# Performance work log

Hardware: AMD Instinct MI355X
Metric: run time of the kernel (lower is better)

## Reference

```python
import jax, jax.numpy as jnp
import numpy as np

EPS = 1e-5

def layernorm(x, w, b):
    m = jnp.mean(x, axis=-1, keepdims=True)
    v = jnp.var(x, axis=-1, keepdims=True)
    return (x - m) * jax.lax.rsqrt(v + EPS) * w + b

def setup_inputs() -> dict:
    key = jax.random.key(0)
    ks = jax.random.split(key, 20)
    B, N, D, H, C = 4, 2048, 512, 8, 3
    HID = int(D * 4.0 * (2.0 / 3.0))  # SwiGLU hidden = 1365
    g = lambda k, shape, s: (jax.random.normal(k, shape, jnp.float32) * s)
    return {
        "x": g(ks[0], (B, N, D), 1.0),
        "coords": jax.random.uniform(ks[1], (B, N, C), jnp.float32),
        "ln1_w": jnp.ones((D,), jnp.float32),
        "ln1_b": jnp.zeros((D,), jnp.float32),
        "ln2_w": jnp.ones((D,), jnp.float32),
        "ln2_b": jnp.zeros((D,), jnp.float32),
        "Wqkv": g(ks[2], (D, 3 * D), D ** -0.5),
        "bqkv": jnp.zeros((3 * D,), jnp.float32),
        "Wo": g(ks[3], (D, D), D ** -0.5),
        "bo": jnp.zeros((D,), jnp.float32),
        "Wc": g(ks[4], (C, H), 0.1),
        "bc": jnp.zeros((H,), jnp.float32),
        "W1": g(ks[5], (D, HID), D ** -0.5),
        "b1": jnp.zeros((HID,), jnp.float32),
        "W2": g(ks[6], (D, HID), D ** -0.5),
        "b2": jnp.zeros((HID,), jnp.float32),
        "W3": g(ks[7], (HID, D), HID ** -0.5),
        "b3": jnp.zeros((D,), jnp.float32),
    }

def reference(x, coords, ln1_w, ln1_b, ln2_w, ln2_b, Wqkv, bqkv, Wo, bo,
              Wc, bc, W1, b1, W2, b2, W3, b3):
    B, N, D = x.shape
    H = bc.shape[0]
    dh = D // H
    # --- coord-aware patch attention (pre-norm) ---
    h = layernorm(x, ln1_w, ln1_b)
    qkv = h @ Wqkv + bqkv                                # [B,N,3D]
    q, k, v = jnp.split(qkv, 3, axis=-1)
    to_heads = lambda t: t.reshape(B, N, H, dh).transpose(0, 2, 1, 3)  # [B,H,N,dh]
    q, k, v = to_heads(q), to_heads(k), to_heads(v)
    scores = jnp.einsum("bhnd,bhmd->bhnm", q, k) / np.sqrt(dh)
    rel = coords[:, :, None, :] - coords[:, None, :, :]  # [B,N,N,C]
    bias = jnp.einsum("bnmc,ch->bhnm", rel, Wc) + bc[None, :, None, None]
    attn = jax.nn.softmax(scores + bias, axis=-1)
    o = jnp.einsum("bhnm,bhmd->bhnd", attn, v)
    o = o.transpose(0, 2, 1, 3).reshape(B, N, D)
    x = x + (o @ Wo + bo)                                # residual 1
    # --- SwiGLU FFN (pre-norm) ---
    h2 = layernorm(x, ln2_w, ln2_b)
    ff = jax.nn.silu(h2 @ W1 + b1) * (h2 @ W2 + b2)
    x = x + (ff @ W3 + b3)                               # residual 2
    return x
```

## Files before the change

kernel.cpp:

```cpp
#include <hip/hip_runtime.h>
#include <hip/hip_bf16.h>
#include <math.h>

#define B_   4
#define N_   2048
#define D_   512
#define H_   8
#define DH_  64
#define C_   3
#define HID_ 1365
#define HIDP 1408
#define ROWS_ (B_*N_)
#define TD_  (3*D_)

typedef __attribute__((ext_vector_type(8))) short short8;
typedef __attribute__((ext_vector_type(4))) float floatx4;
typedef __attribute__((ext_vector_type(2))) unsigned uint2v;

#define MFMA16(a,b,c) __builtin_amdgcn_mfma_f32_16x16x32_bf16(a,b,c,0,0,0)

typedef __attribute__((address_space(3))) unsigned lds_u32;
typedef __attribute__((address_space(1))) unsigned glb_u32;

__device__ __forceinline__ short sh(float v){
  union { __hip_bfloat16 b; short s; } u;
  u.b = __float2bfloat16(v);
  return u.s;
}

__device__ __forceinline__ unsigned pk2(float a, float b){
  union { short s[2]; unsigned u; } z;
  z.s[0] = sh(a); z.s[1] = sh(b);
  return z.u;
}

__device__ __forceinline__ int swz(int col, int row){
  return (col & ~63) | (col & 7) | ((((col >> 3) & 7) ^ (row & 7)) << 3);
}

template<int ROWS, int PITCH, int WAVES = 4>
__device__ __forceinline__ void stageG(short* __restrict__ lds,
    const short* __restrict__ g, int ldg, int t){
  const int LPR = PITCH/8;
  const int RPI = 64/LPR;
  const int PW  = (ROWS/RPI)/WAVES;
  int lane = t & 63, w = t >> 6;
  #pragma unroll
  for (int i = 0; i < PW; ++i){
    int r0  = (w*PW + i)*RPI;
    int row = r0 + lane/LPR;
    const short* ga = g + (size_t)row*ldg + (lane % LPR)*8;
    short* la = lds + r0*PITCH;
    __builtin_amdgcn_global_load_lds((const glb_u32*)ga, (lds_u32*)la, 16, 0, 0);
  }
}

__device__ __forceinline__ short8 fragS(const short* __restrict__ lds, int pitch,
    int mbase, int lane, int kk){
  int row  = mbase + (lane & 15);
  int seg  = (kk >> 3) + (lane >> 4);
  int phys = seg ^ (row & 7);
  return *(const short8*)(lds + row*pitch + phys*8);
}

__global__ __launch_bounds__(256) void convT_all(
    const float* __restrict__ Wqkv, const float* __restrict__ Wo,
    const float* __restrict__ W1, const float* __restrict__ W2,
    const float* __restrict__ W3,
    short* __restrict__ Wtqkv, short* __restrict__ Wto,
    short* __restrict__ Wt1, short* __restrict__ Wt2, short* __restrict__ Wt3,
    const float* __restrict__ coords, const float* __restrict__ Wc,
    float* __restrict__ tv,
    const float* __restrict__ x, const float* __restrict__ ln1_w,
    const float* __restrict__ ln1_b, short* __restrict__ h){
  int id = blockIdx.x;
  int t = threadIdx.x;
  if (id >= 3392){
    int row = id - 3392;
    size_t base = (size_t)row * D_;
    float2 u = *(const float2*)&x[base + 2*t];
    float s  = u.x + u.y;
    float s2 = u.x*u.x + u.y*u.y;
    #pragma unroll
    for (int off = 32; off >= 1; off >>= 1){
      s  += __shfl_xor(s,  off, 64);
      s2 += __shfl_xor(s2, off, 64);
    }
    __shared__ float red[8];
    int lane = t & 63, wv = t >> 6;
    if (lane == 0){ red[wv] = s; red[4+wv] = s2; }
    __syncthreads();
    float sum  = red[0]+red[1]+red[2]+red[3];
    float sum2 = red[4]+red[5]+red[6]+red[7];
    float mean = sum * (1.0f/D_);
    float var  = sum2 * (1.0f/D_) - mean*mean;
    float inv  = rsqrtf(fmaxf(var, 0.f) + 1e-5f);
    float2 wv2 = *(const float2*)&ln1_w[2*t];
    float2 bv2 = *(const float2*)&ln1_b[2*t];
    *(unsigned*)(h + base + swz(2*t, row)) =
        pk2((u.x-mean)*inv*wv2.x + bv2.x, (u.y-mean)*inv*wv2.y + bv2.y);
    return;
  }
  if (id >= 3136){
    int idx = (id - 3136)*256 + t;
    int n = idx & (N_-1);
    int hh = (idx >> 11) & (H_-1);
    int b = idx >> 14;
    float s = 0.f;
    #pragma unroll
    for (int cc = 0; cc < C_; ++cc)
      s += coords[((size_t)(b*N_+n))*C_ + cc] * Wc[cc*H_ + hh];
    tv[idx] = s * 1.44269504f;
    return;
  }
  __shared__ float tile[32][33];
  const float* in; short* out; int K, NN, Kp, nx;
  if (id < 768)      { in=Wqkv; out=Wtqkv; K=512;  NN=1536; Kp=512;  nx=48; }
  else if (id < 1024){ in=Wo;   out=Wto;   K=512;  NN=512;  Kp=512;  nx=16; id-=768; }
  else if (id < 1728){ in=W1;   out=Wt1;   K=512;  NN=HID_; Kp=512;  nx=44; id-=1024; }
  else if (id < 2432){ in=W2;   out=Wt2;   K=512;  NN=HID_; Kp=512;  nx=44; id-=1728; }
  else               { in=W3;   out=Wt3;   K=HID_; NN=512;  Kp=HIDP; nx=16; id-=2432; }
  int nt0 = (id % nx)*32, kt0 = (id / nx)*32;
  int r = t >> 5, cc = t & 31;
  #pragma unroll
  for (int i=0;i<4;++i){
    int k = kt0 + i*8 + r, n = nt0 + cc;
    tile[i*8+r][cc] = (k<K && n<NN) ? in[(size_t)k*NN + n] : 0.f;
  }
  __syncthreads();
  #pragma unroll
  for (int i=0;i<4;++i){
    int n = nt0 + i*8 + r, k = kt0 + cc;
    out[(size_t)n*Kp + swz(k, n)] = sh(tile[cc][i*8+r]);
  }
}

__global__ __launch_bounds__(256) void ln_kernel(const float* __restrict__ x,
        const float* __restrict__ w, const float* __restrict__ b,
        short* __restrict__ out){
  int row = blockIdx.x;
  size_t base = (size_t)row * D_;
  int t = threadIdx.x;
  float2 u = *(const float2*)&x[base + 2*t];
  float s  = u.x + u.y;
  float s2 = u.x*u.x + u.y*u.y;
  #pragma unroll
  for (int off = 32; off >= 1; off >>= 1){
    s  += __shfl_xor(s,  off, 64);
    s2 += __shfl_xor(s2, off, 64);
  }
  __shared__ float red[8];
  int lane = t & 63, wv = t >> 6;
  if (lane == 0){ red[wv] = s; red[4+wv] = s2; }
  __syncthreads();
  float sum  = red[0]+red[1]+red[2]+red[3];
  float sum2 = red[4]+red[5]+red[6]+red[7];
  float mean = sum * (1.0f/D_);
  float var  = sum2 * (1.0f/D_) - mean*mean;
  float inv  = rsqrtf(fmaxf(var, 0.f) + 1e-5f);
  float2 wv2 = *(const float2*)&w[2*t];
  float2 bv2 = *(const float2*)&b[2*t];
  *(unsigned*)(out + base + swz(2*t, row)) =
      pk2((u.x-mean)*inv*wv2.x + bv2.x, (u.y-mean)*inv*wv2.y + bv2.y);
}

__global__ __launch_bounds__(256) void qkv_gemm(
    const short* __restrict__ A, const short* __restrict__ Bt,
    const float* __restrict__ bias,
    short* __restrict__ qb, short* __restrict__ kb, short* __restrict__ vbt){
  __shared__ short As[2][128*64];
  __shared__ short Bs[2][128*64];
  int t = threadIdx.x;
  int lane = t & 63, w = t >> 6;
  int wr = (w >> 1) * 64, wc = (w & 1) * 64;
  int col0 = blockIdx.x * 128, row0 = blockIdx.y * 128;
  bool vblk = (blockIdx.x >= 8);
  floatx4 acc[4][4];
  #pragma unroll
  for (int mt=0;mt<4;++mt)
    #pragma unroll
    for (int nt=0;nt<4;++nt) acc[mt][nt] = (floatx4){0.f,0.f,0.f,0.f};
  stageG<128,64>(As[0], A  + (size_t)row0*D_, D_, t);
  stageG<128,64>(Bs[0], Bt + (size_t)col0*D_, D_, t);
  for (int ti = 0; ti < 8; ++ti){
    int cur = ti & 1;
    __syncthreads();
    if (ti + 1 < 8){
      stageG<128,64>(As[cur^1], A  + (size_t)row0*D_ + (ti+1)*64, D_, t);
      stageG<128,64>(Bs[cur^1], Bt + (size_t)col0*D_ + (ti+1)*64, D_, t);
    }
    #pragma unroll
    for (int kk = 0; kk < 64; kk += 32){
      short8 af[4], bf[4];
      #pragma unroll
      for (int mt=0;mt<4;++mt) af[mt] = fragS(As[cur], 64, wr+mt*16, lane, kk);
      #pragma unroll
      for (int nt=0;nt<4;++nt) bf[nt] = fragS(Bs[cur], 64, wc+nt*16, lane, kk);
      if (vblk){
        #pragma unroll
        for (int mt=0;mt<4;++mt)
          #pragma unroll
          for (int nt=0;nt<4;++nt)
            acc[mt][nt] = MFMA16(af[mt], bf[nt], acc[mt][nt]);
      } else {
        #pragma unroll
        for (int mt=0;mt<4;++mt)
          #pragma unroll
          for (int nt=0;nt<4;++nt)
            acc[mt][nt] = MFMA16(bf[nt], af[mt], acc[mt][nt]);
      }
    }
  }
  int quad = lane >> 4, c = lane & 15;
  if (vblk){
    #pragma unroll
    for (int mt=0;mt<4;++mt){
      int rb0 = row0 + wr + mt*16 + quad*4;
      int bidx = rb0 >> 11, n0 = rb0 & (N_-1);
      #pragma unroll
      for (int nt=0;nt<4;++nt){
        int col = col0 + wc + nt*16 + c;
        int d = col & (D_-1), hh = d >> 6, hd = d & 63;
        float bc = bias[col];
        uint2v pv;
        pv.x = pk2(acc[mt][nt][0]+bc, acc[mt][nt][1]+bc);
        pv.y = pk2(acc[mt][nt][2]+bc, acc[mt][nt][3]+bc);
        *(uint2v*)(vbt + (((size_t)(bidx*H_ + hh))*DH_ + hd)*N_ + swz(n0, hd)) = pv;
      }
    }
  } else {
    #pragma unroll
    for (int mt=0;mt<4;++mt){
      int row = row0 + wr + mt*16 + c;
      int bidx = row >> 11, n = row & (N_-1);
      #pragma unroll
      for (int nt=0;nt<4;++nt){
        int d0 = col0 + wc + nt*16 + quad*4;
        floatx4 b4 = *(const floatx4*)&bias[d0];
        int which = d0 >> 9, dd = d0 & (D_-1), hh = dd >> 6, hd0 = dd & 63;
        short* dst = which ? kb : qb;
        uint2v pv;
        pv.x = pk2(acc[mt][nt][0]+b4[0], acc[mt][nt][1]+b4[1]);
        pv.y = pk2(acc[mt][nt][2]+b4[2], acc[mt][nt][3]+b4[3]);
        *(uint2v*)(dst + (((size_t)(bidx*H_ + hh))*N_ + n)*DH_ + swz(hd0, n)) = pv;
      }
    }
  }
}

__global__ __launch_bounds__(256) void gemm64(
    const short* __restrict__ A, int lda,
    const short* __restrict__ Bt, int Ktot,
    const float* __restrict__ bias,
    const float* __restrict__ resid, float* __restrict__ outF){
  __shared__ short As[2][128*64];
  __shared__ short Bs[2][64*64];
  int t = threadIdx.x, lane = t & 63, w = t >> 6;
  int wr = w * 32;
  int col0 = blockIdx.x * 64, row0 = blockIdx.y * 128;
  floatx4 acc[2][4];
  #pragma unroll
  for (int mt=0;mt<2;++mt)
    #pragma unroll
    for (int nt=0;nt<4;++nt) acc[mt][nt] = (floatx4){0.f,0.f,0.f,0.f};
  stageG<128,64>(As[0], A  + (size_t)row0*lda, lda, t);
  stageG<64,64> (Bs[0], Bt + (size_t)col0*Ktot, Ktot, t);
  const int NT = Ktot >> 6;
  for (int ti = 0; ti < NT; ++ti){
    int cur = ti & 1;
    __syncthreads();
    if (ti + 1 < NT){
      stageG<128,64>(As[cur^1], A  + (size_t)row0*lda + (ti+1)*64, lda, t);
      stageG<64,64> (Bs[cur^1], Bt + (size_t)col0*Ktot + (ti+1)*64, Ktot, t);
    }
    #pragma unroll
    for (int kk = 0; kk < 64; kk += 32){
      short8 af[2], bf[4];
      #pragma unroll
      for (int mt=0;mt<2;++mt) af[mt] = fragS(As[cur], 64, wr+mt*16, lane, kk);
      #pragma unroll
      for (int nt=0;nt<4;++nt) bf[nt] = fragS(Bs[cur], 64, nt*16, lane, kk);
      #pragma unroll
      for (int mt=0;mt<2;++mt)
        #pragma unroll
        for (int nt=0;nt<4;++nt)
          acc[mt][nt] = MFMA16(bf[nt], af[mt], acc[mt][nt]);
    }
  }
  int quad = lane >> 4, c = lane & 15;
  #pragma unroll
  for (int mt=0;mt<2;++mt){
    int row = row0 + wr + mt*16 + c;
    #pragma unroll
    for (int nt=0;nt<4;++nt){
      int c0 = col0 + nt*16 + quad*4;
      size_t idx = (size_t)row*D_ + c0;
      float4 rv = *(const float4*)&resid[idx];
      floatx4 b4 = *(const floatx4*)&bias[c0];
      float4 ov;
      ov.x = acc[mt][nt][0] + b4[0] + rv.x;
      ov.y = acc[mt][nt][1] + b4[1] + rv.y;
      ov.z = acc[mt][nt][2] + b4[2] + rv.z;
      ov.w = acc[mt][nt][3] + b4[3] + rv.w;
      *(float4*)&outF[idx] = ov;
    }
  }
}

__global__ __launch_bounds__(256) void gate_gemm(
    const short* __restrict__ A,
    const short* __restrict__ Bt1, const short* __restrict__ Bt2,
    const float* __restrict__ b1, const float* __restrict__ b2,
    short* __restrict__ ff){
  __shared__ short As[128*64];
  __shared__ short B1s[64*64];
  __shared__ short B2s[64*64];
  int t = threadIdx.x, lane = t & 63, w = t >> 6;
  int wr = (w >> 1) * 64, wc = (w & 1) * 32;
  int col0 = blockIdx.x * 64, row0 = blockIdx.y * 128;
  floatx4 a1[4][2], a2[4][2];
  #pragma unroll
  for (int mt=0;mt<4;++mt)
    #pragma unroll
    for (int nt=0;nt<2;++nt){
      a1[mt][nt] = (floatx4){0.f,0.f,0.f,0.f};
      a2[mt][nt] = (floatx4){0.f,0.f,0.f,0.f};
    }
  for (int k0 = 0; k0 < D_; k0 += 64){
    __syncthreads();
    stageG<128,64>(As, A + (size_t)row0*D_ + k0, D_, t);
    stageG<64,64>(B1s, Bt1 + (size_t)col0*D_ + k0, D_, t);
    stageG<64,64>(B2s, Bt2 + (size_t)col0*D_ + k0, D_, t);
    __syncthreads();
    #pragma unroll
    for (int kk = 0; kk < 64; kk += 32){
      short8 af[4], f1[2], f2[2];
      #pragma unroll
      for (int mt=0;mt<4;++mt) af[mt] = fragS(As, 64, wr+mt*16, lane, kk);
      #pragma unroll
      for (int nt=0;nt<2;++nt){
        f1[nt] = fragS(B1s, 64, wc+nt*16, lane, kk);
        f2[nt] = fragS(B2s, 64, wc+nt*16, lane, kk);
      }
      #pragma unroll
      for (int mt=0;mt<4;++mt)
        #pragma unroll
        for (int nt=0;nt<2;++nt){
          a1[mt][nt] = MFMA16(f1[nt], af[mt], a1[mt][nt]);
          a2[mt][nt] = MFMA16(f2[nt], af[mt], a2[mt][nt]);
        }
    }
  }
  int quad = lane >> 4, c = lane & 15;
  #pragma unroll
  for (int mt=0;mt<4;++mt){
    int row = row0 + wr + mt*16 + c;
    size_t rbase = (size_t)row * HIDP;
    #pragma unroll
    for (int nt=0;nt<2;++nt){
      int c0 = col0 + wc + nt*16 + quad*4;
      float v[4];
      #pragma unroll
      for (int r=0;r<4;++r){
        int col = c0 + r;
        float g1 = a1[mt][nt][r] + (col < HID_ ? b1[col] : 0.f);
        float g2 = a2[mt][nt][r] + (col < HID_ ? b2[col] : 0.f);
        float sig = 1.f / (1.f + __expf(-g1));
        v[r] = g1*sig*g2;
      }
      uint2v pv;
      pv.x = pk2(v[0], v[1]);
      pv.y = pk2(v[2], v[3]);
      *(uint2v*)(ff + rbase + swz(c0, row)) = pv;
    }
  }
}

#define EXP2SC 0.18033688011112042f
__global__ __launch_bounds__(256) void attn_mfma(
    const short* __restrict__ qb, const short* __restrict__ kbuf,
    const short* __restrict__ vbt, const float* __restrict__ tv,
    short* __restrict__ o){
  __shared__ short Ks2[2][128*64];
  __shared__ short Vt2[2][64*128];
  __shared__ __align__(16) float tsAll[2048];
  int qt = blockIdx.x, h = blockIdx.y, b = blockIdx.z;
  int bh = b*H_ + h;
  int t = threadIdx.x, lane = t & 63, w = t >> 6;
  int quad = lane >> 4, c = lane & 15;
  const short* Kbase = kbuf + (size_t)bh*N_*DH_;
  const short* Vbase = vbt  + (size_t)bh*DH_*N_;

  #pragma unroll
  for (int i = 0; i < 2; ++i)
    *(floatx4*)&tsAll[t*8 + i*4] = *(const floatx4*)&tv[(size_t)bh*N_ + t*8 + i*4];
  stageG<128,64>(Ks2[1], qb + ((size_t)bh*N_ + qt*128)*DH_, DH_, t);
  stageG<128,64>(Ks2[0], Kbase, DH_, t);
  stageG<64,128>(Vt2[0], Vbase, N_, t);
  __syncthreads();
  short8 qf[2][2];
  #pragma unroll
  for (int mt=0;mt<2;++mt)
    #pragma unroll
    for (int kh=0;kh<2;++kh)
      qf[mt][kh] = fragS(Ks2[1], 64, w*32 + mt*16, lane, kh*32);
  floatx4 O[2][4];
  float l_i[2] = {0.f, 0.f};
  #pragma unroll
  for (int mt=0;mt<2;++mt)
    #pragma unroll
    for (int nt=0;nt<4;++nt) O[mt][nt] = (floatx4){0.f,0.f,0.f,0.f};
  __syncthreads();

  for (int kt = 0; kt < N_/128; ++kt){
    int cur = kt & 1;
    if (kt + 1 < N_/128){
      stageG<128,64>(Ks2[cur^1], Kbase + (size_t)(kt+1)*128*DH_, DH_, t);
      stageG<64,128>(Vt2[cur^1], Vbase + (kt+1)*128, N_, t);
    }
    const short* Kc  = Ks2[cur];
    const short* Vc  = Vt2[cur];
    const float* tsc = tsAll + kt*128;
    #pragma unroll
    for (int kb4 = 0; kb4 < 4; ++kb4){
      floatx4 St[2][2];
      #pragma unroll
      for (int i=0;i<2;++i){
        St[i][0] = (floatx4){0.f,0.f,0.f,0.f};
        St[i][1] = (floatx4){0.f,0.f,0.f,0.f};
      }
      #pragma unroll
      for (int kh=0;kh<2;++kh){
        short8 kf0 = fragS(Kc, 64, kb4*32,      lane, kh*32);
        short8 kf1 = fragS(Kc, 64, kb4*32 + 16, lane, kh*32);
        #pragma unroll
        for (int mt=0;mt<2;++mt){
          St[0][mt] = MFMA16(kf0, qf[mt][kh], St[0][mt]);
          St[1][mt] = MFMA16(kf1, qf[mt][kh], St[1][mt]);
        }
      }
      floatx4 t0 = *(const floatx4*)&tsc[kb4*32 + quad*4];
      floatx4 t1 = *(const floatx4*)&tsc[kb4*32 + 16 + quad*4];
      short8 pbf[2];
      #pragma unroll
      for (int mt=0;mt<2;++mt){
        float p0[4], p1[4];
        #pragma unroll
        for (int r=0;r<4;++r){
          p0[r] = __builtin_amdgcn_exp2f(fmaf(St[0][mt][r], EXP2SC, -t0[r]));
          p1[r] = __builtin_amdgcn_exp2f(fmaf(St[1][mt][r], EXP2SC, -t1[r]));
        }
        l_i[mt] += (p0[0]+p0[1]) + (p0[2]+p0[3]) + (p1[0]+p1[1]) + (p1[2]+p1[3]);
        unsigned X0 = pk2(p0[0], p0[1]), X1 = pk2(p0[2], p0[3]);
        unsigned Y0 = pk2(p1[0], p1[1]), Y1 = pk2(p1[2], p1[3]);
        auto u0 = __builtin_amdgcn_permlane32_swap(X0, Y0, false, false);
        auto v0 = __builtin_amdgcn_permlane16_swap(u0[0], u0[1], false, false);
        auto u1 = __builtin_amdgcn_permlane32_swap(X1, Y1, false, false);
        auto v1 = __builtin_amdgcn_permlane16_swap(u1[0], u1[1], false, false);
        union { short8 s; unsigned uu[4]; } pb;
        pb.uu[0] = v0[0]; pb.uu[1] = v1[0]; pb.uu[2] = v0[1]; pb.uu[3] = v1[1];
        pbf[mt] = pb.s;
      }
      #pragma unroll
      for (int nt=0;nt<4;++nt){
        short8 vf = fragS(Vc, 128, nt*16, lane, kb4*32);
        #pragma unroll
        for (int mt=0;mt<2;++mt)
          O[mt][nt] = MFMA16(vf, pbf[mt], O[mt][nt]);
      }
    }
    __syncthreads();
  }
  #pragma unroll
  for (int mt=0;mt<2;++mt){
    float l = l_i[mt];
    l += __shfl_xor(l, 16, 64);
    l += __shfl_xor(l, 32, 64);
    float invl = 1.f / l;
    int qrow = qt*128 + w*32 + mt*16 + c;
    size_t rb = ((size_t)b*N_ + qrow)*(size_t)D_;
    #pragma unroll
    for (int nt=0;nt<4;++nt){
      int d0 = h*DH_ + nt*16 + quad*4;
      uint2v pv;
      pv.x = pk2(O[mt][nt][0]*invl, O[mt][nt][1]*invl);
      pv.y = pk2(O[mt][nt][2]*invl, O[mt][nt][3]*invl);
      *(uint2v*)(o + rb + swz(d0, qrow)) = pv;
    }
  }
}

extern "C" void kernel_launch(void* const* d_in, const int* in_sizes, int n_in,
                              void* d_out, int out_size, void* d_ws, size_t ws_size,
                              hipStream_t stream){
  const float* x      = (const float*)d_in[0];
  const float* coords = (const float*)d_in[1];
  const float* ln1_w  = (const float*)d_in[2];
  const float* ln1_b  = (const float*)d_in[3];
  const float* ln2_w  = (const float*)d_in[4];
  const float* ln2_b  = (const float*)d_in[5];
  const float* Wqkv   = (const float*)d_in[6];
  const float* bqkv   = (const float*)d_in[7];
  const float* Wo     = (const float*)d_in[8];
  const float* bo     = (const float*)d_in[9];
  const float* Wc     = (const float*)d_in[10];
  const float* W1     = (const float*)d_in[12];
  const float* b1     = (const float*)d_in[13];
  const float* W2     = (const float*)d_in[14];
  const float* b2     = (const float*)d_in[15];
  const float* W3     = (const float*)d_in[16];
  const float* b3     = (const float*)d_in[17];

  char* ws = (char*)d_ws;
  short* Wtqkv = (short*)(ws);
  short* Wto   = (short*)(ws + 1572864);
  short* Wt1   = (short*)(ws + 2097152);
  short* Wt2   = (short*)(ws + 3538944);
  short* Wt3   = (short*)(ws + 4980736);
  float* tv    = (float*)(ws + 6422528);
  short* h     = (short*)(ws + 6684672);
  short* qb    = (short*)(ws + 15073280);
  short* kb    = (short*)(ws + 23461888);
  short* vbt   = (short*)(ws + 31850496);
  short* o     = h;
  short* h2    = h;
  short* ff    = qb;
  float* x1    = (float*)d_out;

  convT_all<<<dim3(11584), dim3(256), 0, stream>>>(Wqkv, Wo, W1, W2, W3,
      Wtqkv, Wto, Wt1, Wt2, Wt3, coords, Wc, tv, x, ln1_w, ln1_b, h);
  qkv_gemm<<<dim3(12,64), dim3(256), 0, stream>>>(h, Wtqkv, bqkv, qb, kb, vbt);
  attn_mfma<<<dim3(16,8,4), dim3(256), 0, stream>>>(qb, kb, vbt, tv, o);
  gemm64<<<dim3(8,64), dim3(256), 0, stream>>>(o, 512, Wto, 512, bo, x, x1);
  ln_kernel<<<dim3(ROWS_), dim3(256), 0, stream>>>(x1, ln2_w, ln2_b, h2);
  gate_gemm<<<dim3(22,64), dim3(256), 0, stream>>>(h2, Wt1, Wt2, b1, b2, ff);
  gemm64<<<dim3(8,64), dim3(256), 0, stream>>>(ff, HIDP, Wt3, HIDP, b3, x1, x1);
}
```

Baseline: 305.1 us.

## Remap workgroups for XCD-local L2 reuse and software-pipeline attention QK/PV

Flattens the launch grids of the QKV, output, gate and W3 GEMMs and of attention into 1D, then remaps block IDs so that consecutive tiles sharing rows or heads land on the same XCD. The intent is better L2 reuse across MI355X's per-XCD caches. The attention inner loop is also restructured to interleave the QK^T MFMAs of the next 32-key sub-block with the softmax/PV of the current one, so MFMA work overlaps exp and permute work. This raises live register pressure through two S accumulator sets.

After: 277.2 us. 1.1x faster.

```diff
diff --git a/kernel.cpp b/kernel.cpp
--- a/kernel.cpp
+++ b/kernel.cpp
@@ -36,6 +36,10 @@
 
 __device__ __forceinline__ int swz(int col, int row){
   return (col & ~63) | (col & 7) | ((((col >> 3) & 7) ^ (row & 7)) << 3);
+}
+
+__device__ __forceinline__ int xcdswz(int bid, int nwg){
+  return (bid & 7) * (nwg >> 3) + (bid >> 3);
 }
 
 template<int ROWS, int PITCH, int WAVES = 4>
@@ -173,8 +177,10 @@
   int t = threadIdx.x;
   int lane = t & 63, w = t >> 6;
   int wr = (w >> 1) * 64, wc = (w & 1) * 64;
-  int col0 = blockIdx.x * 128, row0 = blockIdx.y * 128;
-  bool vblk = (blockIdx.x >= 8);
+  int wg = xcdswz(blockIdx.x, 768);
+  int colblk = wg % 12, rowblk = wg / 12;
+  int col0 = colblk * 128, row0 = rowblk * 128;
+  bool vblk = (colblk >= 8);
   floatx4 acc[4][4];
   #pragma unroll
   for (int mt=0;mt<4;++mt)
@@ -257,7 +263,8 @@
   __shared__ short Bs[2][64*64];
   int t = threadIdx.x, lane = t & 63, w = t >> 6;
   int wr = w * 32;
-  int col0 = blockIdx.x * 64, row0 = blockIdx.y * 128;
+  int wg = xcdswz(blockIdx.x, 512);
+  int col0 = (wg & 7) * 64, row0 = (wg >> 3) * 128;
   floatx4 acc[2][4];
   #pragma unroll
   for (int mt=0;mt<2;++mt)
@@ -317,7 +324,8 @@
   __shared__ short B2s[64*64];
   int t = threadIdx.x, lane = t & 63, w = t >> 6;
   int wr = (w >> 1) * 64, wc = (w & 1) * 32;
-  int col0 = blockIdx.x * 64, row0 = blockIdx.y * 128;
+  int wg = xcdswz(blockIdx.x, 1408);
+  int col0 = (wg % 22) * 64, row0 = (wg / 22) * 128;
   floatx4 a1[4][2], a2[4][2];
   #pragma unroll
   for (int mt=0;mt<4;++mt)
@@ -377,6 +385,54 @@
 }
 
 #define EXP2SC 0.18033688011112042f
+
+#define ZERO_S(S) { \
+  S[0][0] = (floatx4){0.f,0.f,0.f,0.f}; S[0][1] = (floatx4){0.f,0.f,0.f,0.f}; \
+  S[1][0] = (floatx4){0.f,0.f,0.f,0.f}; S[1][1] = (floatx4){0.f,0.f,0.f,0.f}; }
+
+#define QKT(S, kb) { \
+  _Pragma("unroll") \
+  for (int kh=0;kh<2;++kh){ \
+    short8 kf0 = fragS(Kc, 64, (kb)*32,      lane, kh*32); \
+    short8 kf1 = fragS(Kc, 64, (kb)*32 + 16, lane, kh*32); \
+    _Pragma("unroll") \
+    for (int mt=0;mt<2;++mt){ \
+      S[0][mt] = MFMA16(kf0, qf[mt][kh], S[0][mt]); \
+      S[1][mt] = MFMA16(kf1, qf[mt][kh], S[1][mt]); \
+    } \
+  } }
+
+#define SOFTPV(S, kb) { \
+  floatx4 t0 = *(const floatx4*)&tsc[(kb)*32 + quad*4]; \
+  floatx4 t1 = *(const floatx4*)&tsc[(kb)*32 + 16 + quad*4]; \
+  short8 pbf[2]; \
+  _Pragma("unroll") \
+  for (int mt=0;mt<2;++mt){ \
+    float p0[4], p1[4]; \
+    _Pragma("unroll") \
+    for (int r=0;r<4;++r){ \
+      p0[r] = __builtin_amdgcn_exp2f(fmaf(S[0][mt][r], EXP2SC, -t0[r])); \
+      p1[r] = __builtin_amdgcn_exp2f(fmaf(S[1][mt][r], EXP2SC, -t1[r])); \
+    } \
+    l_i[mt] += (p0[0]+p0[1]) + (p0[2]+p0[3]) + (p1[0]+p1[1]) + (p1[2]+p1[3]); \
+    unsigned X0 = pk2(p0[0], p0[1]), X1 = pk2(p0[2], p0[3]); \
+    unsigned Y0 = pk2(p1[0], p1[1]), Y1 = pk2(p1[2], p1[3]); \
+    auto u0 = __builtin_amdgcn_permlane32_swap(X0, Y0, false, false); \
+    auto v0 = __builtin_amdgcn_permlane16_swap(u0[0], u0[1], false, false); \
+    auto u1 = __builtin_amdgcn_permlane32_swap(X1, Y1, false, false); \
+    auto v1 = __builtin_amdgcn_permlane16_swap(u1[0], u1[1], false, false); \
+    union { short8 s; unsigned uu[4]; } pb; \
+    pb.uu[0] = v0[0]; pb.uu[1] = v1[0]; pb.uu[2] = v0[1]; pb.uu[3] = v1[1]; \
+    pbf[mt] = pb.s; \
+  } \
+  _Pragma("unroll") \
+  for (int nt=0;nt<4;++nt){ \
+    short8 vf = fragS(Vc, 128, nt*16, lane, (kb)*32); \
+    _Pragma("unroll") \
+    for (int mt=0;mt<2;++mt) \
+      O[mt][nt] = MFMA16(vf, pbf[mt], O[mt][nt]); \
+  } }
+
 __global__ __launch_bounds__(256) void attn_mfma(
     const short* __restrict__ qb, const short* __restrict__ kbuf,
     const short* __restrict__ vbt, const float* __restrict__ tv,
@@ -384,8 +440,9 @@
   __shared__ short Ks2[2][128*64];
   __shared__ short Vt2[2][64*128];
   __shared__ __align__(16) float tsAll[2048];
-  int qt = blockIdx.x, h = blockIdx.y, b = blockIdx.z;
-  int bh = b*H_ + h;
+  int wg = xcdswz(blockIdx.x, 512);
+  int bh = wg >> 4, qt = wg & 15;
+  int b = bh >> 3, h = bh & 7;
   int t = threadIdx.x, lane = t & 63, w = t >> 6;
   int quad = lane >> 4, c = lane & 15;
   const short* Kbase = kbuf + (size_t)bh*N_*DH_;
@@ -421,54 +478,15 @@
     const short* Kc  = Ks2[cur];
     const short* Vc  = Vt2[cur];
     const float* tsc = tsAll + kt*128;
-    #pragma unroll
-    for (int kb4 = 0; kb4 < 4; ++kb4){
-      floatx4 St[2][2];
-      #pragma unroll
-      for (int i=0;i<2;++i){
-        St[i][0] = (floatx4){0.f,0.f,0.f,0.f};
-        St[i][1] = (floatx4){0.f,0.f,0.f,0.f};
-      }
-      #pragma unroll
-      for (int kh=0;kh<2;++kh){
-        short8 kf0 = fragS(Kc, 64, kb4*32,      lane, kh*32);
-        short8 kf1 = fragS(Kc, 64, kb4*32 + 16, lane, kh*32);
-        #pragma unroll
-        for (int mt=0;mt<2;++mt){
-          St[0][mt] = MFMA16(kf0, qf[mt][kh], St[0][mt]);
-          St[1][mt] = MFMA16(kf1, qf[mt][kh], St[1][mt]);
-        }
-      }
-      floatx4 t0 = *(const floatx4*)&tsc[kb4*32 + quad*4];
-      floatx4 t1 = *(const floatx4*)&tsc[kb4*32 + 16 + quad*4];
-      short8 pbf[2];
-      #pragma unroll
-      for (int mt=0;mt<2;++mt){
-        float p0[4], p1[4];
-        #pragma unroll
-        for (int r=0;r<4;++r){
-          p0[r] = __builtin_amdgcn_exp2f(fmaf(St[0][mt][r], EXP2SC, -t0[r]));
-          p1[r] = __builtin_amdgcn_exp2f(fmaf(St[1][mt][r], EXP2SC, -t1[r]));
-        }
-        l_i[mt] += (p0[0]+p0[1]) + (p0[2]+p0[3]) + (p1[0]+p1[1]) + (p1[2]+p1[3]);
-        unsigned X0 = pk2(p0[0], p0[1]), X1 = pk2(p0[2], p0[3]);
-        unsigned Y0 = pk2(p1[0], p1[1]), Y1 = pk2(p1[2], p1[3]);
-        auto u0 = __builtin_amdgcn_permlane32_swap(X0, Y0, false, false);
-        auto v0 = __builtin_amdgcn_permlane16_swap(u0[0], u0[1], false, false);
-        auto u1 = __builtin_amdgcn_permlane32_swap(X1, Y1, false, false);
-        auto v1 = __builtin_amdgcn_permlane16_swap(u1[0], u1[1], false, false);
-        union { short8 s; unsigned uu[4]; } pb;
-        pb.uu[0] = v0[0]; pb.uu[1] = v1[0]; pb.uu[2] = v0[1]; pb.uu[3] = v1[1];
-        pbf[mt] = pb.s;
-      }
-      #pragma unroll
-      for (int nt=0;nt<4;++nt){
-        short8 vf = fragS(Vc, 128, nt*16, lane, kb4*32);
-        #pragma unroll
-        for (int mt=0;mt<2;++mt)
-          O[mt][nt] = MFMA16(vf, pbf[mt], O[mt][nt]);
-      }
-    }
+    floatx4 Sa[2][2], Sb[2][2];
+    ZERO_S(Sa); QKT(Sa, 0);
+    ZERO_S(Sb); QKT(Sb, 1);
+    SOFTPV(Sa, 0);
+    ZERO_S(Sa); QKT(Sa, 2);
+    SOFTPV(Sb, 1);
+    ZERO_S(Sb); QKT(Sb, 3);
+    SOFTPV(Sa, 2);
+    SOFTPV(Sb, 3);
     __syncthreads();
   }
   #pragma unroll
@@ -529,10 +547,10 @@
 
   convT_all<<<dim3(11584), dim3(256), 0, stream>>>(Wqkv, Wo, W1, W2, W3,
       Wtqkv, Wto, Wt1, Wt2, Wt3, coords, Wc, tv, x, ln1_w, ln1_b, h);
-  qkv_gemm<<<dim3(12,64), dim3(256), 0, stream>>>(h, Wtqkv, bqkv, qb, kb, vbt);
-  attn_mfma<<<dim3(16,8,4), dim3(256), 0, stream>>>(qb, kb, vbt, tv, o);
-  gemm64<<<dim3(8,64), dim3(256), 0, stream>>>(o, 512, Wto, 512, bo, x, x1);
+  qkv_gemm<<<dim3(768), dim3(256), 0, stream>>>(h, Wtqkv, bqkv, qb, kb, vbt);
+  attn_mfma<<<dim3(512), dim3(256), 0, stream>>>(qb, kb, vbt, tv, o);
+  gemm64<<<dim3(512), dim3(256), 0, stream>>>(o, 512, Wto, 512, bo, x, x1);
   ln_kernel<<<dim3(ROWS_), dim3(256), 0, stream>>>(x1, ln2_w, ln2_b, h2);
-  gate_gemm<<<dim3(22,64), dim3(256), 0, stream>>>(h2, Wt1, Wt2, b1, b2, ff);
-  gemm64<<<dim3(8,64), dim3(256), 0, stream>>>(ff, HIDP, Wt3, HIDP, b3, x1, x1);
-}
+  gate_gemm<<<dim3(1408), dim3(256), 0, stream>>>(h2, Wt1, Wt2, b1, b2, ff);
+  gemm64<<<dim3(512), dim3(256), 0, stream>>>(ff, HIDP, Wt3, HIDP, b3, x1, x1);
+}
```
